# Kernel tuning notes

Hardware: AMD Instinct MI355X
Metric: run time of the kernel (lower is better)

The kernel has to match this reference:

```python
import jax, jax.numpy as jnp
import numpy as np

E = 2048        # embedding_dim
H = 16          # num_q_heads
G = 4           # group_size
HKV = H // G    # num_kv_heads = 4
D = E // H      # q_head_dim = 128
KVD = E // G    # kv_head_dim = 512
B, N = 2, 2048


def setup_inputs() -> dict:
    key = jax.random.key(0)
    ks = jax.random.split(key, 5)
    s = 0.02
    return {
        "x": jax.random.normal(ks[0], (B, N, E), jnp.float32),
        "Wq": jax.random.normal(ks[1], (E, E), jnp.float32) * s,
        "Wk": jax.random.normal(ks[2], (KVD, E), jnp.float32) * s,
        "Wv": jax.random.normal(ks[3], (KVD, E), jnp.float32) * s,
        "Wo": jax.random.normal(ks[4], (E, E), jnp.float32) * s,
    }


def reference(x, Wq, Wk, Wv, Wo):
    b, n, _ = x.shape
    # projections (nn.Linear: y = x @ W.T)
    q = x @ Wq.T                              # (b, n, E)
    k = x @ Wk.T                              # (b, n, KVD)
    v = x @ Wv.T                              # (b, n, KVD)
    # split heads: q -> b h n d with h=H, then (h g) -> g,h layout
    q = q.reshape(b, n, H, D).transpose(0, 2, 1, 3)          # b H n d
    q = q.reshape(b, HKV, G, n, D).transpose(0, 2, 1, 3, 4)  # b g h n d  (h=HKV)
    k = k.reshape(b, n, HKV, D).transpose(0, 2, 1, 3)        # b h s d
    v = v.reshape(b, n, HKV, D).transpose(0, 2, 1, 3)        # b h s d
    scale = 1.0 / jnp.sqrt(jnp.asarray(D, x.dtype))
    scores = jnp.einsum('bghnd,bhsd->bghns', q, k) * scale   # full score tensor
    scores = jax.nn.softmax(scores, axis=-1)
    # dropout p=0.0 -> identity
    o = jnp.einsum('bghns,bhsd->bghnd', scores, v)           # b g h n d
    # rearrange 'b g h n d -> b n (h g) d' then concat heads
    o = o.transpose(0, 3, 2, 1, 4).reshape(b, n, E)          # b n (h g) d -> b n E
    return o @ Wo.T
```

## Files before the change

kernel.cpp:

```cpp
#include <hip/hip_runtime.h>
#include <hip/hip_bf16.h>
#include <cstdint>
#include <cstddef>

using u16 = unsigned short;
typedef __bf16 bf16x8 __attribute__((ext_vector_type(8)));
typedef float f32x4 __attribute__((ext_vector_type(4)));
typedef float f32x16 __attribute__((ext_vector_type(16)));
typedef u16 u16x4 __attribute__((ext_vector_type(4)));
typedef u16 u16x8 __attribute__((ext_vector_type(8)));
typedef uint32_t u32x2 __attribute__((ext_vector_type(2)));
typedef uint32_t u32x4 __attribute__((ext_vector_type(4)));

__device__ __forceinline__ u16 f2bf(float f) {
  uint32_t u = __builtin_bit_cast(uint32_t, f);
  u += 0x7FFFu + ((u >> 16) & 1u);
  return (u16)(u >> 16);
}

__device__ __forceinline__ void gld_lds16(const void* g, void* l) {
  __builtin_amdgcn_global_load_lds(
      (const __attribute__((address_space(1))) unsigned int*)g,
      (__attribute__((address_space(3))) unsigned int*)l, 16, 0, 0);
}

#define MFMA16(a, b, c) __builtin_amdgcn_mfma_f32_16x16x32_bf16((a), (b), (c), 0, 0, 0)
#define MFMA32(a, b, c) __builtin_amdgcn_mfma_f32_32x32x16_bf16((a), (b), (c), 0, 0, 0)

__device__ __forceinline__ uint32_t pkbf(float a, float b) {
  uint32_t d;
  asm("v_cvt_pk_bf16_f32 %0, %1, %2" : "=v"(d) : "v"(a), "v"(b));
  return d;
}
__device__ __forceinline__ void swap32(uint32_t& a, uint32_t& b) {
  asm volatile("v_permlane32_swap_b32 %0, %1" : "+v"(a), "+v"(b));
}
__device__ __forceinline__ bf16x8 mk8(u32x2 a, u32x2 b) {
  return __builtin_bit_cast(bf16x8, u32x4{a[0], a[1], b[0], b[1]});
}

__global__ void cvt_kernel(const float* __restrict__ in, u16* __restrict__ out, int n4) {
  int i = blockIdx.x * blockDim.x + threadIdx.x;
  int stride = gridDim.x * blockDim.x;
  for (; i < n4; i += stride) {
    float4 v = reinterpret_cast<const float4*>(in)[i];
    u16x4 o;
    o[0] = f2bf(v.x); o[1] = f2bf(v.y); o[2] = f2bf(v.z); o[3] = f2bf(v.w);
    reinterpret_cast<u16x4*>(out)[i] = o;
  }
}

__global__ void cvt4_kernel(const float* __restrict__ x, const float* __restrict__ Wq,
                            const float* __restrict__ Wk, const float* __restrict__ Wv,
                            u16* __restrict__ xb, u16* __restrict__ Wc) {
  int i = blockIdx.x * blockDim.x + threadIdx.x;
  int stride = gridDim.x * blockDim.x;
  for (; i < 3670016; i += stride) {
    const float* src; u16* dst; int off;
    if (i < 2097152)      { src = x;  dst = xb;            off = i; }
    else if (i < 3145728) { src = Wq; dst = Wc;            off = i - 2097152; }
    else if (i < 3407872) { src = Wk; dst = Wc + 4194304;  off = i - 3145728; }
    else                  { src = Wv; dst = Wc + 5242880;  off = i - 3407872; }
    float4 v = reinterpret_cast<const float4*>(src)[off];
    u16x4 o;
    o[0] = f2bf(v.x); o[1] = f2bf(v.y); o[2] = f2bf(v.z); o[3] = f2bf(v.w);
    reinterpret_cast<u16x4*>(dst)[off] = o;
  }
}

template <bool OUT_BF16>
__global__ __launch_bounds__(256) void gemm_bt(const u16* __restrict__ A,
                                               const u16* __restrict__ B,
                                               void* __restrict__ Cv,
                                               int M, int N, int K) {
  __shared__ __align__(16) u16 Ash[3][128 * 32];
  __shared__ __align__(16) u16 Bsh[3][128 * 32];
  const int tid = threadIdx.x;
  const int w = tid >> 6, lane = tid & 63, ql = lane & 15, g = lane >> 4;
  const int wr = w >> 1, wc = w & 1;
  const int bid = blockIdx.y * gridDim.x + blockIdx.x;
  const int nwg = gridDim.x * gridDim.y;
  const int wg = (bid & 7) * (nwg >> 3) + (bid >> 3);
  const int m0 = (wg / gridDim.x) * 128, n0 = (wg % gridDim.x) * 128;
  const int srow = w * 16 + (lane >> 2);
  const int sk = (lane & 3) * 8;
  const u16* Abase = A + (size_t)(m0 + srow) * K + sk;
  const u16* Bbase = B + (size_t)(n0 + srow) * K + sk;

  f32x4 acc[4][4];
#pragma unroll
  for (int i = 0; i < 4; i++)
#pragma unroll
    for (int j = 0; j < 4; j++) acc[i][j] = f32x4{0.f, 0.f, 0.f, 0.f};

  auto stage = [&](int bi, int tile) {
    const int kt = tile * 32;
    gld_lds16(Abase + kt,                  &Ash[bi][w * 512]);
    gld_lds16(Abase + (size_t)64 * K + kt, &Ash[bi][2048 + w * 512]);
    gld_lds16(Bbase + kt,                  &Bsh[bi][w * 512]);
    gld_lds16(Bbase + (size_t)64 * K + kt, &Bsh[bi][2048 + w * 512]);
  };

  const int nt = K >> 5;
  stage(0, 0);
  stage(1, 1);
  asm volatile("s_waitcnt vmcnt(4)" ::: "memory");
  __builtin_amdgcn_sched_barrier(0);
  __builtin_amdgcn_s_barrier();
  __builtin_amdgcn_sched_barrier(0);

  int cur = 0;
  for (int t = 0; t < nt; ++t) {
    if (t + 2 < nt) {
      int stg = cur + 2; if (stg >= 3) stg -= 3;
      stage(stg, t + 2);
    }
    bf16x8 af[4], bfr[4];
#pragma unroll
    for (int i = 0; i < 4; i++)
      af[i] = *reinterpret_cast<const bf16x8*>(&Ash[cur][(wr * 64 + i * 16 + ql) * 32 + g * 8]);
#pragma unroll
    for (int j = 0; j < 4; j++)
      bfr[j] = *reinterpret_cast<const bf16x8*>(&Bsh[cur][(wc * 64 + j * 16 + ql) * 32 + g * 8]);
    __builtin_amdgcn_s_setprio(1);
#pragma unroll
    for (int i = 0; i < 4; i++)
#pragma unroll
      for (int j = 0; j < 4; j++)
        acc[i][j] = MFMA16(af[i], bfr[j], acc[i][j]);
    __builtin_amdgcn_s_setprio(0);
    if (t + 1 < nt) {
      if (t + 2 < nt) {
        asm volatile("s_waitcnt vmcnt(4)" ::: "memory");
      } else {
        asm volatile("s_waitcnt vmcnt(0)" ::: "memory");
      }
      __builtin_amdgcn_sched_barrier(0);
      __builtin_amdgcn_s_barrier();
      __builtin_amdgcn_sched_barrier(0);
    }
    cur = (cur == 2) ? 0 : cur + 1;
  }

#pragma unroll
  for (int i = 0; i < 4; i++)
#pragma unroll
    for (int j = 0; j < 4; j++)
#pragma unroll
      for (int r = 0; r < 4; r++) {
        const int row = m0 + wr * 64 + i * 16 + g * 4 + r;
        const int col = n0 + wc * 64 + j * 16 + ql;
        if constexpr (OUT_BF16)
          ((u16*)Cv)[(size_t)row * N + col] = f2bf(acc[i][j][r]);
        else
          ((float*)Cv)[(size_t)row * N + col] = acc[i][j][r];
      }
}

#define TRRD(D, B, IMM) \
  asm volatile("ds_read_b64_tr_b16 %0, %1 offset:" #IMM : "=v"(D) : "v"(B))

#define PV_CLUSTER(PF, O0, O1, O2, O3, O4, O5, O6, O7)                          \
  do {                                                                          \
    u32x2 a0, a1, b0, b1, c0, c1, d0, d1;                                       \
    TRRD(a0, ab, O0); TRRD(a1, ab, O1); TRRD(b0, ab, O2); TRRD(b1, ab, O3);     \
    TRRD(c0, ab, O4); TRRD(c1, ab, O5); TRRD(d0, ab, O6); TRRD(d1, ab, O7);     \
    asm volatile("s_waitcnt lgkmcnt(0)" ::: "memory");                          \
    __builtin_amdgcn_sched_barrier(0);                                          \
    __builtin_amdgcn_s_setprio(1);                                              \
    oacc[0] = MFMA32(PF, mk8(a0, a1), oacc[0]);                                 \
    oacc[1] = MFMA32(PF, mk8(b0, b1), oacc[1]);                                 \
    oacc[2] = MFMA32(PF, mk8(c0, c1), oacc[2]);                                 \
    oacc[3] = MFMA32(PF, mk8(d0, d1), oacc[3]);                                 \
    __builtin_amdgcn_s_setprio(0);                                              \
  } while (0)

__global__ __launch_bounds__(256, 2) void attn_kernel(const u16* __restrict__ QKV,
                                                      u16* __restrict__ O) {
  __shared__ __align__(16) u16 SHK[2 * 8192];
  __shared__ __align__(16) u16 SHV[2 * 8320];
  __shared__ float lbuf[4][32];
  const int tid = threadIdx.x, w = tid >> 6, lane = tid & 63;
  const int lq = lane & 31, hi = lane >> 5;
  const int bid = blockIdx.x;
  const int swz = (bid & 7) * 64 + (bid >> 3);
  const int qt = swz & 15;
  const int bh = swz >> 4;
  const int b = bh >> 4, h = bh & 15, hkv = h >> 2;
  const size_t rowb = (size_t)b * 2048;
  const int qbase = qt * 128 + w * 32;

  const u16* Kg = QKV + 2048 + hkv * 128;
  const u16* Vg = QKV + 2560 + hkv * 128;

  bf16x8 bq[8];
  {
    const u16* qp = QKV + (rowb + qbase + lq) * 3072 + h * 128 + hi * 8;
#pragma unroll
    for (int s5 = 0; s5 < 8; s5++)
      bq[s5] = *reinterpret_cast<const bf16x8*>(qp + s5 * 16);
  }

  f32x16 oacc[4], lacc;
#pragma unroll
  for (int dt = 0; dt < 4; dt++)
#pragma unroll
    for (int i = 0; i < 16; i++) oacc[dt][i] = 0.f;
#pragma unroll
  for (int i = 0; i < 16; i++) lacc[i] = 0.f;
  const float CEXP = 0.08838834764831845f * 1.4426950408889634f;

  const bf16x8 ones = __builtin_bit_cast(bf16x8,
      u32x4{0x3F803F80u, 0x3F803F80u, 0x3F803F80u, 0x3F803F80u});

  auto stageK = [&](int pb2, int sbase) {
#pragma unroll
    for (int p = 0; p < 4; p++) {
      const int L = p * 2048 + tid * 8;
      const int s = L >> 7;
      const int gI = (L >> 3) & 15;
      gld_lds16(Kg + (rowb + sbase + s) * 3072 + ((gI ^ (s & 7)) << 3),
                &SHK[pb2 * 8192 + p * 2048 + w * 512]);
    }
  };
  auto stageV = [&](int pb2, int sbase) {
#pragma unroll
    for (int c = 0; c < 4; c++) {
      const int idx = w * 4 + c;
      const int dg = idx >> 1, half = idx & 1;
      const int s = half * 32 + (lane >> 1);
      const int dr0 = (lane & 1) * 8;
      gld_lds16(Vg + (rowb + sbase + s) * 3072 + dg * 16 + dr0,
                &SHV[pb2 * 8320 + dg * 1040 + half * 512]);
    }
  };

#define KFRAG(PB, SH, S5) \
  (*reinterpret_cast<const bf16x8*>(&SHK[(PB)*8192 + ((SH)*32 + lq) * 128 + ((((S5)*2 + hi) ^ (lq & 7)) << 3)]))

  const uint32_t vbase0 =
      (uint32_t)(uintptr_t)(__attribute__((address_space(3))) u16*)&SHV[0];
  const uint32_t vlane = vbase0 + ((lane >> 4) & 1) * 2080u + (lane >> 5) * 256u
                       + (lane & 15) * 8u;

  stageK(0, 0);
  stageV(0, 0);
  __syncthreads();

#pragma unroll 1
  for (int sb = 0; sb < 32; sb++) {
    const int pb = sb & 1;
    if (sb < 31) {
      stageK(pb ^ 1, (sb + 1) * 64);
      stageV(pb ^ 1, (sb + 1) * 64);
    }

    f32x16 sc0, sc1;
#pragma unroll
    for (int i = 0; i < 16; i++) { sc0[i] = 0.f; sc1[i] = 0.f; }
    __builtin_amdgcn_s_setprio(1);
#pragma unroll
    for (int s5 = 0; s5 < 8; s5++) {
      sc0 = MFMA32(KFRAG(pb, 0, s5), bq[s5], sc0);
      sc1 = MFMA32(KFRAG(pb, 1, s5), bq[s5], sc1);
    }
    __builtin_amdgcn_s_setprio(0);

    float e0[16], e1[16];
#pragma unroll
    for (int i = 0; i < 16; i++) {
      e0[i] = exp2f(sc0[i] * CEXP);
      e1[i] = exp2f(sc1[i] * CEXP);
    }
    bf16x8 pf0, pf1, pf2, pf3;
    {
      uint32_t a, bw;
      u32x4 f;
      a = pkbf(e0[0], e0[1]);  bw = pkbf(e0[4], e0[5]);  swap32(a, bw);
      f[0] = a; f[2] = bw;
      a = pkbf(e0[2], e0[3]);  bw = pkbf(e0[6], e0[7]);  swap32(a, bw);
      f[1] = a; f[3] = bw;
      pf0 = __builtin_bit_cast(bf16x8, f);
      a = pkbf(e0[8], e0[9]);  bw = pkbf(e0[12], e0[13]); swap32(a, bw);
      f[0] = a; f[2] = bw;
      a = pkbf(e0[10], e0[11]); bw = pkbf(e0[14], e0[15]); swap32(a, bw);
      f[1] = a; f[3] = bw;
      pf1 = __builtin_bit_cast(bf16x8, f);
      a = pkbf(e1[0], e1[1]);  bw = pkbf(e1[4], e1[5]);  swap32(a, bw);
      f[0] = a; f[2] = bw;
      a = pkbf(e1[2], e1[3]);  bw = pkbf(e1[6], e1[7]);  swap32(a, bw);
      f[1] = a; f[3] = bw;
      pf2 = __builtin_bit_cast(bf16x8, f);
      a = pkbf(e1[8], e1[9]);  bw = pkbf(e1[12], e1[13]); swap32(a, bw);
      f[0] = a; f[2] = bw;
      a = pkbf(e1[10], e1[11]); bw = pkbf(e1[14], e1[15]); swap32(a, bw);
      f[1] = a; f[3] = bw;
      pf3 = __builtin_bit_cast(bf16x8, f);
    }

    lacc = MFMA32(ones, pf0, lacc);
    lacc = MFMA32(ones, pf1, lacc);
    lacc = MFMA32(ones, pf2, lacc);
    lacc = MFMA32(ones, pf3, lacc);

    {
      const uint32_t ab = vlane + (uint32_t)(pb * 16640);
      PV_CLUSTER(pf0, 0, 128, 4160, 4288, 8320, 8448, 12480, 12608);
      PV_CLUSTER(pf1, 512, 640, 4672, 4800, 8832, 8960, 12992, 13120);
      PV_CLUSTER(pf2, 1024, 1152, 5184, 5312, 9344, 9472, 13504, 13632);
      PV_CLUSTER(pf3, 1536, 1664, 5696, 5824, 9856, 9984, 14016, 14144);
    }

    __syncthreads();
  }

  if (hi == 0) lbuf[w][lq] = lacc[0];
  __syncthreads();
  u16* ob = (w < 2) ? &SHK[w * 8192] : &SHV[(w - 2) * 8320];
#pragma unroll
  for (int dt = 0; dt < 4; dt++)
#pragma unroll
    for (int r = 0; r < 16; r++) {
      const int qr = (r & 3) + 8 * (r >> 2) + 4 * hi;
      ob[qr * 136 + dt * 32 + lq] = f2bf(oacc[dt][r] * (1.0f / lbuf[w][qr]));
    }
  const int orow = lane >> 1, och = (lane & 1) * 64;
  u16* og = O + (rowb + qbase + orow) * 2048 + h * 128 + och;
#pragma unroll
  for (int t = 0; t < 8; t++) {
    u16x8 v = *reinterpret_cast<const u16x8*>(&ob[orow * 136 + och + t * 8]);
    *reinterpret_cast<u16x8*>(og + t * 8) = v;
  }
#undef KFRAG
}

extern "C" void kernel_launch(void* const* d_in, const int* in_sizes, int n_in,
                              void* d_out, int out_size, void* d_ws, size_t ws_size,
                              hipStream_t stream) {
  (void)in_sizes; (void)n_in; (void)out_size;
  const float* x  = (const float*)d_in[0];
  const float* Wq = (const float*)d_in[1];
  const float* Wk = (const float*)d_in[2];
  const float* Wv = (const float*)d_in[3];
  const float* Wo = (const float*)d_in[4];

  if (ws_size < (size_t)(8388608 + 6291456 + 12582912) * 2) return;
  u16* xb  = (u16*)d_ws;
  u16* Wc  = xb + 8388608;
  u16* QKV = Wc + 6291456;
  u16* Ob  = xb;

  cvt4_kernel<<<2048, 256, 0, stream>>>(x, Wq, Wk, Wv, xb, Wc);
  gemm_bt<true><<<dim3(24, 32), 256, 0, stream>>>(xb, Wc, (void*)QKV, 4096, 3072, 2048);
  cvt_kernel<<<2048, 256, 0, stream>>>(Wo, Wc, 1048576);
  attn_kernel<<<dim3(512), 256, 0, stream>>>(QKV, Ob);
  gemm_bt<false><<<dim3(16, 32), 256, 0, stream>>>(Ob, Wc, d_out, 4096, 2048, 2048);
}
```

Baseline: 224.1 us.

## Switch attention loop to 32-key tiles with triple-buffered async LDS staging

The key/value tile per iteration is halved from 64 to 32 rows and the LDS ring grows from two to three buffers. Loads are issued two tiles ahead, and each iteration waits on vmcnt counts instead of a full syncthreads, which should let global loads overlap more compute. In exchange the loop runs twice as many iterations, each doing half the MFMA work, so barrier and loop overhead per unit of work goes up. The epilogue output buffer offsets are recomputed to fit the smaller shared arrays.

```diff
diff --git a/kernel.cpp b/kernel.cpp
--- a/kernel.cpp
+++ b/kernel.cpp
@@ -177,8 +177,8 @@
 
 __global__ __launch_bounds__(256, 2) void attn_kernel(const u16* __restrict__ QKV,
                                                       u16* __restrict__ O) {
-  __shared__ __align__(16) u16 SHK[2 * 8192];
-  __shared__ __align__(16) u16 SHV[2 * 8320];
+  __shared__ __align__(16) u16 SHK[3 * 4096];
+  __shared__ __align__(16) u16 SHV[3 * 4160];
   __shared__ float lbuf[4][32];
   const int tid = threadIdx.x, w = tid >> 6, lane = tid & 63;
   const int lq = lane & 31, hi = lane >> 5;
@@ -213,110 +213,107 @@
   const bf16x8 ones = __builtin_bit_cast(bf16x8,
       u32x4{0x3F803F80u, 0x3F803F80u, 0x3F803F80u, 0x3F803F80u});
 
-  auto stageK = [&](int pb2, int sbase) {
-#pragma unroll
-    for (int p = 0; p < 4; p++) {
+  auto stageK = [&](int kb, int sbase) {
+#pragma unroll
+    for (int p = 0; p < 2; p++) {
       const int L = p * 2048 + tid * 8;
       const int s = L >> 7;
       const int gI = (L >> 3) & 15;
       gld_lds16(Kg + (rowb + sbase + s) * 3072 + ((gI ^ (s & 7)) << 3),
-                &SHK[pb2 * 8192 + p * 2048 + w * 512]);
+                &SHK[kb * 4096 + p * 2048 + w * 512]);
     }
   };
-  auto stageV = [&](int pb2, int sbase) {
-#pragma unroll
-    for (int c = 0; c < 4; c++) {
-      const int idx = w * 4 + c;
-      const int dg = idx >> 1, half = idx & 1;
-      const int s = half * 32 + (lane >> 1);
+  auto stageV = [&](int vb, int sbase) {
+#pragma unroll
+    for (int c = 0; c < 2; c++) {
+      const int dg = w * 2 + c;
+      const int s = lane >> 1;
       const int dr0 = (lane & 1) * 8;
       gld_lds16(Vg + (rowb + sbase + s) * 3072 + dg * 16 + dr0,
-                &SHV[pb2 * 8320 + dg * 1040 + half * 512]);
+                &SHV[vb * 4160 + dg * 520]);
     }
   };
 
-#define KFRAG(PB, SH, S5) \
-  (*reinterpret_cast<const bf16x8*>(&SHK[(PB)*8192 + ((SH)*32 + lq) * 128 + ((((S5)*2 + hi) ^ (lq & 7)) << 3)]))
+#define KFRAG(PB, S5) \
+  (*reinterpret_cast<const bf16x8*>(&SHK[(PB)*4096 + lq * 128 + ((((S5)*2 + hi) ^ (lq & 7)) << 3)]))
 
   const uint32_t vbase0 =
       (uint32_t)(uintptr_t)(__attribute__((address_space(3))) u16*)&SHV[0];
-  const uint32_t vlane = vbase0 + ((lane >> 4) & 1) * 2080u + (lane >> 5) * 256u
+  const uint32_t vlane = vbase0 + ((lane >> 4) & 1) * 1040u + (lane >> 5) * 256u
                        + (lane & 15) * 8u;
 
   stageK(0, 0);
   stageV(0, 0);
-  __syncthreads();
-
+  stageK(1, 32);
+  stageV(1, 32);
+  asm volatile("s_waitcnt vmcnt(4)" ::: "memory");
+  __builtin_amdgcn_sched_barrier(0);
+  __builtin_amdgcn_s_barrier();
+  __builtin_amdgcn_sched_barrier(0);
+
+  int cur = 0;
 #pragma unroll 1
-  for (int sb = 0; sb < 32; sb++) {
-    const int pb = sb & 1;
-    if (sb < 31) {
-      stageK(pb ^ 1, (sb + 1) * 64);
-      stageV(pb ^ 1, (sb + 1) * 64);
-    }
-
-    f32x16 sc0, sc1;
-#pragma unroll
-    for (int i = 0; i < 16; i++) { sc0[i] = 0.f; sc1[i] = 0.f; }
+  for (int t = 0; t < 64; ++t) {
+    if (t + 2 < 64) {
+      int stg = cur + 2; if (stg >= 3) stg -= 3;
+      stageK(stg, (t + 2) * 32);
+      stageV(stg, (t + 2) * 32);
+    }
+
+    f32x16 sc;
+#pragma unroll
+    for (int i = 0; i < 16; i++) sc[i] = 0.f;
     __builtin_amdgcn_s_setprio(1);
 #pragma unroll
-    for (int s5 = 0; s5 < 8; s5++) {
-      sc0 = MFMA32(KFRAG(pb, 0, s5), bq[s5], sc0);
-      sc1 = MFMA32(KFRAG(pb, 1, s5), bq[s5], sc1);
-    }
+    for (int s5 = 0; s5 < 8; s5++)
+      sc = MFMA32(KFRAG(cur, s5), bq[s5], sc);
     __builtin_amdgcn_s_setprio(0);
 
-    float e0[16], e1[16];
-#pragma unroll
-    for (int i = 0; i < 16; i++) {
-      e0[i] = exp2f(sc0[i] * CEXP);
-      e1[i] = exp2f(sc1[i] * CEXP);
-    }
-    bf16x8 pf0, pf1, pf2, pf3;
+    float e[16];
+#pragma unroll
+    for (int i = 0; i < 16; i++) e[i] = exp2f(sc[i] * CEXP);
+    bf16x8 pf0, pf1;
     {
       uint32_t a, bw;
       u32x4 f;
-      a = pkbf(e0[0], e0[1]);  bw = pkbf(e0[4], e0[5]);  swap32(a, bw);
+      a = pkbf(e[0], e[1]);   bw = pkbf(e[4], e[5]);   swap32(a, bw);
       f[0] = a; f[2] = bw;
-      a = pkbf(e0[2], e0[3]);  bw = pkbf(e0[6], e0[7]);  swap32(a, bw);
+      a = pkbf(e[2], e[3]);   bw = pkbf(e[6], e[7]);   swap32(a, bw);
       f[1] = a; f[3] = bw;
       pf0 = __builtin_bit_cast(bf16x8, f);
-      a = pkbf(e0[8], e0[9]);  bw = pkbf(e0[12], e0[13]); swap32(a, bw);
+      a = pkbf(e[8], e[9]);   bw = pkbf(e[12], e[13]); swap32(a, bw);
       f[0] = a; f[2] = bw;
-      a = pkbf(e0[10], e0[11]); bw = pkbf(e0[14], e0[15]); swap32(a, bw);
+      a = pkbf(e[10], e[11]); bw = pkbf(e[14], e[15]); swap32(a, bw);
       f[1] = a; f[3] = bw;
       pf1 = __builtin_bit_cast(bf16x8, f);
-      a = pkbf(e1[0], e1[1]);  bw = pkbf(e1[4], e1[5]);  swap32(a, bw);
-      f[0] = a; f[2] = bw;
-      a = pkbf(e1[2], e1[3]);  bw = pkbf(e1[6], e1[7]);  swap32(a, bw);
-      f[1] = a; f[3] = bw;
-      pf2 = __builtin_bit_cast(bf16x8, f);
-      a = pkbf(e1[8], e1[9]);  bw = pkbf(e1[12], e1[13]); swap32(a, bw);
-      f[0] = a; f[2] = bw;
-      a = pkbf(e1[10], e1[11]); bw = pkbf(e1[14], e1[15]); swap32(a, bw);
-      f[1] = a; f[3] = bw;
-      pf3 = __builtin_bit_cast(bf16x8, f);
     }
 
     lacc = MFMA32(ones, pf0, lacc);
     lacc = MFMA32(ones, pf1, lacc);
-    lacc = MFMA32(ones, pf2, lacc);
-    lacc = MFMA32(ones, pf3, lacc);
 
     {
-      const uint32_t ab = vlane + (uint32_t)(pb * 16640);
-      PV_CLUSTER(pf0, 0, 128, 4160, 4288, 8320, 8448, 12480, 12608);
-      PV_CLUSTER(pf1, 512, 640, 4672, 4800, 8832, 8960, 12992, 13120);
-      PV_CLUSTER(pf2, 1024, 1152, 5184, 5312, 9344, 9472, 13504, 13632);
-      PV_CLUSTER(pf3, 1536, 1664, 5696, 5824, 9856, 9984, 14016, 14144);
-    }
-
-    __syncthreads();
-  }
+      const uint32_t ab = vlane + (uint32_t)(cur * 8320);
+      PV_CLUSTER(pf0, 0, 128, 2080, 2208, 4160, 4288, 6240, 6368);
+      PV_CLUSTER(pf1, 512, 640, 2592, 2720, 4672, 4800, 6752, 6880);
+    }
+
+    if (t + 1 < 64) {
+      if (t + 2 < 64) {
+        asm volatile("s_waitcnt vmcnt(4)" ::: "memory");
+      } else {
+        asm volatile("s_waitcnt vmcnt(0)" ::: "memory");
+      }
+      __builtin_amdgcn_sched_barrier(0);
+      __builtin_amdgcn_s_barrier();
+      __builtin_amdgcn_sched_barrier(0);
+    }
+    cur = (cur == 2) ? 0 : cur + 1;
+  }
+  __syncthreads();
 
   if (hi == 0) lbuf[w][lq] = lacc[0];
   __syncthreads();
-  u16* ob = (w < 2) ? &SHK[w * 8192] : &SHV[(w - 2) * 8320];
+  u16* ob = (w < 2) ? &SHK[w * 4352] : &SHV[(w - 2) * 4352];
 #pragma unroll
   for (int dt = 0; dt < 4; dt++)
 #pragma unroll
```

Result: slower. 232.7 us (+3.8%).
